# Kernel tuning notes

Hardware: AMD Instinct MI355X
Metric: run time of the kernel (lower is better)

Reference implementation:

```python
import jax, jax.numpy as jnp
import numpy as np

N_ENV = 100000
D_PS = 512
N_SPECIES = 4
N_SUPPORT = 256
N_STRUCT = 1000
ZETA = 2


def setup_inputs() -> dict:
    key = jax.random.key(0)
    k1, k2, k3, k4, k5 = jax.random.split(key, 5)
    power_spectrum = jax.random.normal(k1, (N_ENV, D_PS), dtype=jnp.float32)
    sp = jax.random.normal(k2, (N_SPECIES, N_SUPPORT, D_PS), dtype=jnp.float32)
    # CosineKernel asserts support points are unit-norm
    support_points = sp / jnp.linalg.norm(sp, axis=-1, keepdims=True)
    weights = jax.random.normal(k3, (N_SPECIES, 1, N_SUPPORT), dtype=jnp.float32)
    all_species = jax.random.randint(k4, (N_ENV,), 0, N_SPECIES, dtype=jnp.int64)
    structure_ids = jnp.sort(jax.random.randint(k5, (N_ENV,), 0, N_STRUCT, dtype=jnp.int64))
    return {
        "power_spectrum": power_spectrum,
        "support_points": support_points,
        "weights": weights,
        "all_species": all_species,
        "structure_ids": structure_ids,
    }


def reference(power_spectrum, support_points, weights, all_species, structure_ids):
    # Normalize each environment's power spectrum (CosineKernel)
    ps = power_spectrum / jnp.linalg.norm(power_spectrum, axis=1, keepdims=True)
    # Kernel of every environment against every species' support set: [N, S, M]
    k = jnp.einsum("nd,smd->nsm", ps, support_points) ** ZETA
    # Per-row energy contribution for each species: k @ weights[s].T -> [N, S]
    contrib = jnp.einsum("nsm,sm->ns", k, weights[:, 0, :])
    # Species masking: each row only contributes through its own species' kernel
    onehot = jax.nn.one_hot(all_species, N_SPECIES, dtype=contrib.dtype)  # [N, S]
    per_row = jnp.sum(contrib * onehot, axis=1)  # [N]
    # Segmented sum over structures (equivalent to looping over structures_slices)
    energy = jax.ops.segment_sum(per_row, structure_ids, num_segments=N_STRUCT)
    return energy[:, None]  # [n_structures, 1]
```

## Files before the change

kernel.cpp:

```cpp
#include <hip/hip_runtime.h>
#include <hip/hip_bf16.h>


constexpr int kNEnv     = 100000;
constexpr int kDPS      = 512;
constexpr int kNSpecies = 4;
constexpr int kNSupport = 256;
constexpr int kCap      = 32768;

constexpr int BN = 128;
constexpr int BM = 128;
constexpr int BK = 32;
constexpr int LDSS = 40;

typedef __attribute__((ext_vector_type(8))) short short8;
typedef __attribute__((ext_vector_type(4))) float f32x4;

__global__ void scatter_kernel(const int* __restrict__ species, const int* __restrict__ sid,
                               int* __restrict__ cnt, int* __restrict__ perm,
                               int* __restrict__ sidp) {
  __shared__ int lcnt[kNSpecies];
  __shared__ int lbase[kNSpecies];
  int t = threadIdx.x;
  if (t < kNSpecies) lcnt[t] = 0;
  __syncthreads();
  int i = blockIdx.x * 256 + t;
  bool v = i < kNEnv;
  int s = 0, r = 0, g = 0;
  if (v) { s = species[i]; r = atomicAdd(&lcnt[s], 1); g = sid[i]; }
  __syncthreads();
  if (t < kNSpecies) lbase[t] = lcnt[t] ? atomicAdd(&cnt[t], lcnt[t]) : 0;
  __syncthreads();
  if (v) {
    int d = s * kCap + lbase[s] + r;
    perm[d] = i;
    sidp[d] = g;
  }
}

__device__ inline short8 pack_bf16x8(const float4& a, const float4& b) {
  union { short8 v; __hip_bfloat162 h[4]; } u;
  u.h[0] = __float22bfloat162_rn({a.x, a.y});
  u.h[1] = __float22bfloat162_rn({a.z, a.w});
  u.h[2] = __float22bfloat162_rn({b.x, b.y});
  u.h[3] = __float22bfloat162_rn({b.z, b.w});
  return u.v;
}

__global__ __launch_bounds__(256) void gap_gemm_kernel(
    const float* __restrict__ ps, const float* __restrict__ sp,
    const float* __restrict__ w, const int* __restrict__ cnt,
    const int* __restrict__ perm, const int* __restrict__ sidp,
    float* __restrict__ energy) {
  const int s     = blockIdx.z;
  const int count = min(cnt[s], kCap);
  const int tile0 = blockIdx.x * BN;
  if (tile0 >= count) return;
  const int m0    = blockIdx.y * BM;

  __shared__ short a_sh[BN * LDSS];
  __shared__ short b_sh[BM * LDSS];
  __shared__ float red[4][64];
  __shared__ float sqs[2][BN];

  const int tid  = threadIdx.x;
  const int wv   = tid >> 6;
  const int lane = tid & 63;

  const int st_r = tid & 127;
  const int st_p = tid >> 7;

  const int ge   = tile0 + st_r;
  const int arow = perm[s * kCap + (ge < count ? ge : count - 1)];
  const float* a_src = ps + (size_t)arow * kDPS + st_p * 16;
  const float* b_src = sp + ((size_t)s * kNSupport + m0 + st_r) * kDPS + st_p * 16;
  const float* w_s   = w + s * kNSupport;

  const int wv_e = (wv & 1) * 64;
  const int wv_m = (wv >> 1) * 64;
  const int l15  = lane & 15;
  const int lq   = lane >> 4;

  float wgt[4];
  #pragma unroll
  for (int fj = 0; fj < 4; ++fj) wgt[fj] = w_s[m0 + wv_m + fj * 16 + l15];

  f32x4 acc[4][4];
  #pragma unroll
  for (int i = 0; i < 4; ++i)
    #pragma unroll
    for (int j = 0; j < 4; ++j) acc[i][j] = (f32x4)0.f;

  float sqsum = 0.f;

  float4 va[4], vb[4];
  #pragma unroll
  for (int j = 0; j < 4; ++j) {
    va[j] = *(const float4*)(a_src + j * 4);
    vb[j] = *(const float4*)(b_src + j * 4);
  }

  for (int k0 = 0; k0 < kDPS; k0 += BK) {
    __syncthreads();
    #pragma unroll
    for (int j = 0; j < 4; ++j)
      sqsum += va[j].x * va[j].x + va[j].y * va[j].y + va[j].z * va[j].z + va[j].w * va[j].w;
    {
      short* ap = &a_sh[st_r * LDSS + st_p * 16];
      *(short8*)(ap)     = pack_bf16x8(va[0], va[1]);
      *(short8*)(ap + 8) = pack_bf16x8(va[2], va[3]);
      short* bp = &b_sh[st_r * LDSS + st_p * 16];
      *(short8*)(bp)     = pack_bf16x8(vb[0], vb[1]);
      *(short8*)(bp + 8) = pack_bf16x8(vb[2], vb[3]);
    }
    __syncthreads();
    if (k0 + BK < kDPS) {
      #pragma unroll
      for (int j = 0; j < 4; ++j) {
        va[j] = *(const float4*)(a_src + k0 + BK + j * 4);
        vb[j] = *(const float4*)(b_src + k0 + BK + j * 4);
      }
    }
    short8 af[4], bf[4];
    #pragma unroll
    for (int fi = 0; fi < 4; ++fi)
      af[fi] = *(const short8*)&a_sh[(wv_e + fi * 16 + l15) * LDSS + lq * 8];
    #pragma unroll
    for (int fj = 0; fj < 4; ++fj)
      bf[fj] = *(const short8*)&b_sh[(wv_m + fj * 16 + l15) * LDSS + lq * 8];
    #pragma unroll
    for (int fi = 0; fi < 4; ++fi)
      #pragma unroll
      for (int fj = 0; fj < 4; ++fj)
        acc[fi][fj] = __builtin_amdgcn_mfma_f32_16x16x32_bf16(af[fi], bf[fj], acc[fi][fj], 0, 0, 0);
  }

  sqs[st_p][st_r] = sqsum;

  #pragma unroll
  for (int fi = 0; fi < 4; ++fi) {
    #pragma unroll
    for (int r = 0; r < 4; ++r) {
      float p = 0.f;
      #pragma unroll
      for (int fj = 0; fj < 4; ++fj) {
        float c = acc[fi][fj][r];
        p += c * c * wgt[fj];
      }
      p += __shfl_xor(p, 1, 64);
      p += __shfl_xor(p, 2, 64);
      p += __shfl_xor(p, 4, 64);
      p += __shfl_xor(p, 8, 64);
      if (l15 == 0) red[wv][fi * 16 + lq * 4 + r] = p;
    }
  }
  __syncthreads();
  if (tid < BN) {
    int h = tid >> 6, el = tid & 63;
    int row = h * 64 + el;
    float v = red[h][el] + red[h + 2][el];
    int g = tile0 + row;
    if (g < count) {
      float inv = 1.0f / (sqs[0][row] + sqs[1][row]);
      atomicAdd(&energy[sidp[s * kCap + g]], v * inv);
    }
  }
}

extern "C" void kernel_launch(void* const* d_in, const int* in_sizes, int n_in,
                              void* d_out, int out_size, void* d_ws, size_t ws_size,
                              hipStream_t stream) {
  const float* ps      = (const float*)d_in[0];
  const float* sp      = (const float*)d_in[1];
  const float* w       = (const float*)d_in[2];
  const int*   species = (const int*)d_in[3];
  const int*   sid     = (const int*)d_in[4];
  float* energy = (float*)d_out;

  char* wsb = (char*)d_ws;
  int* cnt  = (int*)wsb;
  int* perm = (int*)(wsb + 256);
  int* sidp = (int*)(wsb + 256 + 4 * kCap * sizeof(int));

  hipMemsetAsync(cnt, 0, 16, stream);
  hipMemsetAsync(energy, 0, out_size * sizeof(float), stream);

  scatter_kernel<<<(kNEnv + 255) / 256, 256, 0, stream>>>(species, sid, cnt, perm, sidp);

  dim3 grid(kCap / BN, kNSupport / BM, kNSpecies);
  gap_gemm_kernel<<<grid, 256, 0, stream>>>(ps, sp, w, cnt, perm, sidp, energy);
}
```

Before: 403.8 us.

## Pre-convert support points to bf16 and load MFMA fragments directly from global

The scatter kernel now also converts the support points to bf16 once, into a workspace buffer. The GEMM kernel covers all 256 support points per block (BM=256), so the environment rows are read and normalised only once instead of twice. LDS staging and the block barriers are gone: each lane loads its A and B fragments straight from global memory, and each wave holds 4x8 accumulators. This cuts global reads and synchronisation, but it raises register pressure, drops explicit prefetch double-buffering, and makes the loads less coalesced.

Result: slower. 630.8 us (+56.2%).

```diff
diff --git a/kernel.cpp b/kernel.cpp
--- a/kernel.cpp
+++ b/kernel.cpp
@@ -9,36 +9,13 @@
 constexpr int kCap      = 32768;
 
 constexpr int BN = 128;
-constexpr int BM = 128;
+constexpr int BM = 256;
 constexpr int BK = 32;
-constexpr int LDSS = 40;
 
 typedef __attribute__((ext_vector_type(8))) short short8;
 typedef __attribute__((ext_vector_type(4))) float f32x4;
 
-__global__ void scatter_kernel(const int* __restrict__ species, const int* __restrict__ sid,
-                               int* __restrict__ cnt, int* __restrict__ perm,
-                               int* __restrict__ sidp) {
-  __shared__ int lcnt[kNSpecies];
-  __shared__ int lbase[kNSpecies];
-  int t = threadIdx.x;
-  if (t < kNSpecies) lcnt[t] = 0;
-  __syncthreads();
-  int i = blockIdx.x * 256 + t;
-  bool v = i < kNEnv;
-  int s = 0, r = 0, g = 0;
-  if (v) { s = species[i]; r = atomicAdd(&lcnt[s], 1); g = sid[i]; }
-  __syncthreads();
-  if (t < kNSpecies) lbase[t] = lcnt[t] ? atomicAdd(&cnt[t], lcnt[t]) : 0;
-  __syncthreads();
-  if (v) {
-    int d = s * kCap + lbase[s] + r;
-    perm[d] = i;
-    sidp[d] = g;
-  }
-}
-
-__device__ inline short8 pack_bf16x8(const float4& a, const float4& b) {
+__device__ __forceinline__ short8 pack_bf16x8(const float4& a, const float4& b) {
   union { short8 v; __hip_bfloat162 h[4]; } u;
   u.h[0] = __float22bfloat162_rn({a.x, a.y});
   u.h[1] = __float22bfloat162_rn({a.z, a.w});
@@ -47,8 +24,39 @@
   return u.v;
 }
 
+__global__ void scatter_convert_kernel(const float* __restrict__ sp,
+                                       const int* __restrict__ species,
+                                       const int* __restrict__ sid,
+                                       int* __restrict__ cnt, int* __restrict__ perm,
+                                       int* __restrict__ sidp, short* __restrict__ spb) {
+  const int t = threadIdx.x;
+  const int b = blockIdx.x;
+  if (b < (kNSpecies * kNSupport * kDPS) / (256 * 8)) {
+    const int base = (b * 256 + t) * 8;
+    const float4 lo = *(const float4*)(sp + base);
+    const float4 hi = *(const float4*)(sp + base + 4);
+    *(short8*)(spb + base) = pack_bf16x8(lo, hi);
+  }
+  __shared__ int lcnt[kNSpecies];
+  __shared__ int lbase[kNSpecies];
+  if (t < kNSpecies) lcnt[t] = 0;
+  __syncthreads();
+  const int i = b * 256 + t;
+  const bool v = i < kNEnv;
+  int s = 0, r = 0, g = 0;
+  if (v) { s = species[i]; r = atomicAdd(&lcnt[s], 1); g = sid[i]; }
+  __syncthreads();
+  if (t < kNSpecies) lbase[t] = lcnt[t] ? atomicAdd(&cnt[t], lcnt[t]) : 0;
+  __syncthreads();
+  if (v) {
+    const int d = s * kCap + lbase[s] + r;
+    perm[d] = i;
+    sidp[d] = g;
+  }
+}
+
 __global__ __launch_bounds__(256) void gap_gemm_kernel(
-    const float* __restrict__ ps, const float* __restrict__ sp,
+    const float* __restrict__ ps, const short* __restrict__ spb,
     const float* __restrict__ w, const int* __restrict__ cnt,
     const int* __restrict__ perm, const int* __restrict__ sidp,
     float* __restrict__ energy) {
@@ -56,86 +64,69 @@
   const int count = min(cnt[s], kCap);
   const int tile0 = blockIdx.x * BN;
   if (tile0 >= count) return;
-  const int m0    = blockIdx.y * BM;
 
-  __shared__ short a_sh[BN * LDSS];
-  __shared__ short b_sh[BM * LDSS];
   __shared__ float red[4][64];
-  __shared__ float sqs[2][BN];
+  __shared__ float sqs[BN];
 
   const int tid  = threadIdx.x;
   const int wv   = tid >> 6;
   const int lane = tid & 63;
-
-  const int st_r = tid & 127;
-  const int st_p = tid >> 7;
-
-  const int ge   = tile0 + st_r;
-  const int arow = perm[s * kCap + (ge < count ? ge : count - 1)];
-  const float* a_src = ps + (size_t)arow * kDPS + st_p * 16;
-  const float* b_src = sp + ((size_t)s * kNSupport + m0 + st_r) * kDPS + st_p * 16;
-  const float* w_s   = w + s * kNSupport;
-
-  const int wv_e = (wv & 1) * 64;
-  const int wv_m = (wv >> 1) * 64;
   const int l15  = lane & 15;
   const int lq   = lane >> 4;
+  const int wv_e = (wv & 1) * 64;
+  const int wv_m = (wv >> 1) * 128;
 
-  float wgt[4];
+  const float* aptr[4];
   #pragma unroll
-  for (int fj = 0; fj < 4; ++fj) wgt[fj] = w_s[m0 + wv_m + fj * 16 + l15];
-
-  f32x4 acc[4][4];
+  for (int fi = 0; fi < 4; ++fi) {
+    const int ge   = tile0 + wv_e + fi * 16 + l15;
+    const int arow = perm[s * kCap + (ge < count ? ge : count - 1)];
+    aptr[fi] = ps + (size_t)arow * kDPS + lq * 8;
+  }
+  const short* bptr[8];
+  float wgt[8];
+  const float* w_s = w + s * kNSupport;
   #pragma unroll
-  for (int i = 0; i < 4; ++i)
-    #pragma unroll
-    for (int j = 0; j < 4; ++j) acc[i][j] = (f32x4)0.f;
-
-  float sqsum = 0.f;
-
-  float4 va[4], vb[4];
-  #pragma unroll
-  for (int j = 0; j < 4; ++j) {
-    va[j] = *(const float4*)(a_src + j * 4);
-    vb[j] = *(const float4*)(b_src + j * 4);
+  for (int fj = 0; fj < 8; ++fj) {
+    const int m = wv_m + fj * 16 + l15;
+    bptr[fj] = spb + ((size_t)s * kNSupport + m) * kDPS + lq * 8;
+    wgt[fj]  = w_s[m];
   }
 
+  f32x4 acc[4][8];
+  #pragma unroll
+  for (int fi = 0; fi < 4; ++fi)
+    #pragma unroll
+    for (int fj = 0; fj < 8; ++fj) acc[fi][fj] = (f32x4)0.f;
+  float sq[4] = {0.f, 0.f, 0.f, 0.f};
+
+  #pragma unroll
   for (int k0 = 0; k0 < kDPS; k0 += BK) {
-    __syncthreads();
+    short8 bf[8];
     #pragma unroll
-    for (int j = 0; j < 4; ++j)
-      sqsum += va[j].x * va[j].x + va[j].y * va[j].y + va[j].z * va[j].z + va[j].w * va[j].w;
-    {
-      short* ap = &a_sh[st_r * LDSS + st_p * 16];
-      *(short8*)(ap)     = pack_bf16x8(va[0], va[1]);
-      *(short8*)(ap + 8) = pack_bf16x8(va[2], va[3]);
-      short* bp = &b_sh[st_r * LDSS + st_p * 16];
-      *(short8*)(bp)     = pack_bf16x8(vb[0], vb[1]);
-      *(short8*)(bp + 8) = pack_bf16x8(vb[2], vb[3]);
+    for (int fj = 0; fj < 8; ++fj) bf[fj] = *(const short8*)(bptr[fj] + k0);
+    #pragma unroll
+    for (int fi = 0; fi < 4; ++fi) {
+      const float4 lo = *(const float4*)(aptr[fi] + k0);
+      const float4 hi = *(const float4*)(aptr[fi] + k0 + 4);
+      sq[fi] += lo.x * lo.x + lo.y * lo.y + lo.z * lo.z + lo.w * lo.w
+              + hi.x * hi.x + hi.y * hi.y + hi.z * hi.z + hi.w * hi.w;
+      const short8 af = pack_bf16x8(lo, hi);
+      #pragma unroll
+      for (int fj = 0; fj < 8; ++fj)
+        acc[fi][fj] = __builtin_amdgcn_mfma_f32_16x16x32_bf16(af, bf[fj], acc[fi][fj], 0, 0, 0);
     }
-    __syncthreads();
-    if (k0 + BK < kDPS) {
-      #pragma unroll
-      for (int j = 0; j < 4; ++j) {
-        va[j] = *(const float4*)(a_src + k0 + BK + j * 4);
-        vb[j] = *(const float4*)(b_src + k0 + BK + j * 4);
-      }
-    }
-    short8 af[4], bf[4];
-    #pragma unroll
-    for (int fi = 0; fi < 4; ++fi)
-      af[fi] = *(const short8*)&a_sh[(wv_e + fi * 16 + l15) * LDSS + lq * 8];
-    #pragma unroll
-    for (int fj = 0; fj < 4; ++fj)
-      bf[fj] = *(const short8*)&b_sh[(wv_m + fj * 16 + l15) * LDSS + lq * 8];
-    #pragma unroll
-    for (int fi = 0; fi < 4; ++fi)
-      #pragma unroll
-      for (int fj = 0; fj < 4; ++fj)
-        acc[fi][fj] = __builtin_amdgcn_mfma_f32_16x16x32_bf16(af[fi], bf[fj], acc[fi][fj], 0, 0, 0);
   }
 
-  sqs[st_p][st_r] = sqsum;
+  if (wv < 2) {
+    #pragma unroll
+    for (int fi = 0; fi < 4; ++fi) {
+      float p = sq[fi];
+      p += __shfl_xor(p, 16, 64);
+      p += __shfl_xor(p, 32, 64);
+      if (lane < 16) sqs[wv_e + fi * 16 + lane] = p;
+    }
+  }
 
   #pragma unroll
   for (int fi = 0; fi < 4; ++fi) {
@@ -143,8 +134,8 @@
     for (int r = 0; r < 4; ++r) {
       float p = 0.f;
       #pragma unroll
-      for (int fj = 0; fj < 4; ++fj) {
-        float c = acc[fi][fj][r];
+      for (int fj = 0; fj < 8; ++fj) {
+        const float c = acc[fi][fj][r];
         p += c * c * wgt[fj];
       }
       p += __shfl_xor(p, 1, 64);
@@ -156,14 +147,10 @@
   }
   __syncthreads();
   if (tid < BN) {
-    int h = tid >> 6, el = tid & 63;
-    int row = h * 64 + el;
-    float v = red[h][el] + red[h + 2][el];
-    int g = tile0 + row;
-    if (g < count) {
-      float inv = 1.0f / (sqs[0][row] + sqs[1][row]);
-      atomicAdd(&energy[sidp[s * kCap + g]], v * inv);
-    }
+    const int h  = tid >> 6, el = tid & 63;
+    const float v = red[h][el] + red[h + 2][el];
+    const int g  = tile0 + h * 64 + el;
+    if (g < count) atomicAdd(&energy[sidp[s * kCap + g]], v / sqs[h * 64 + el]);
   }
 }
 
@@ -177,16 +164,18 @@
   const int*   sid     = (const int*)d_in[4];
   float* energy = (float*)d_out;
 
-  char* wsb = (char*)d_ws;
-  int* cnt  = (int*)wsb;
-  int* perm = (int*)(wsb + 256);
-  int* sidp = (int*)(wsb + 256 + 4 * kCap * sizeof(int));
+  char* wsb  = (char*)d_ws;
+  int*   cnt  = (int*)wsb;
+  int*   perm = (int*)(wsb + 256);
+  int*   sidp = (int*)(wsb + 256 + 4 * kCap * sizeof(int));
+  short* spb  = (short*)(wsb + 256 + 8 * kCap * sizeof(int));
 
   hipMemsetAsync(cnt, 0, 16, stream);
   hipMemsetAsync(energy, 0, out_size * sizeof(float), stream);
 
-  scatter_kernel<<<(kNEnv + 255) / 256, 256, 0, stream>>>(species, sid, cnt, perm, sidp);
+  scatter_convert_kernel<<<(kNEnv + 255) / 256, 256, 0, stream>>>(
+      sp, species, sid, cnt, perm, sidp, spb);
 
-  dim3 grid(kCap / BN, kNSupport / BM, kNSpecies);
-  gap_gemm_kernel<<<grid, 256, 0, stream>>>(ps, sp, w, cnt, perm, sidp, energy);
+  dim3 grid(kCap / BN, 1, kNSpecies);
+  gap_gemm_kernel<<<grid, 256, 0, stream>>>(ps, spb, w, cnt, perm, sidp, energy);
 }
```
